# Kernel optimization log

Measured on AMD Instinct MI355X. Metric: run time of the kernel, lower is better.

## Reference

```python
import jax, jax.numpy as jnp
import numpy as np

WIN = 16
HEADS = 8


def _rel_index(win):
    c = np.stack(np.meshgrid(np.arange(win), np.arange(win), indexing='ij'), 0).reshape(2, -1)
    rel = (c[:, :, None] - c[:, None, :]).transpose(1, 2, 0) + win - 1
    return jnp.asarray(rel[..., 0] * (2 * win - 1) + rel[..., 1])


def setup_inputs() -> dict:
    key = jax.random.key(0)
    ks = jax.random.split(key, 10)
    B, H, W, C = 4, 128, 128, 256
    f = lambda k, s: jax.random.normal(k, s, dtype=jnp.float32)
    return {
        'x_wsa': f(ks[0], (B, H, W, C)),
        'x_original': f(ks[1], (B, H, W, C)),
        'q_w': f(ks[2], (C, C)) * 0.02,
        'q_b': f(ks[3], (C,)) * 0.02,
        'kv_w': f(ks[4], (5, 5, C // HEADS, 2 * C)) * 0.02,  # HWIO, grouped conv
        'kv_b': f(ks[5], (2 * C,)) * 0.02,
        'out_w': f(ks[6], (C, C)) * 0.02,
        'out_b': f(ks[7], (C,)) * 0.02,
        'bias_table': f(ks[8], ((2 * WIN - 1) ** 2, HEADS)) * 0.02,
        'rezero': jnp.full((1,), 0.5, dtype=jnp.float32),  # nonzero so output is informative
    }


def reference(x_wsa, x_original, q_w, q_b, kv_w, kv_b, out_w, out_b, bias_table, rezero):
    B, H, W, C = x_wsa.shape
    win, h = WIN, HEADS
    d = C // h
    nH, nW = H // win, W // win

    q = x_wsa @ q_w + q_b  # [B,H,W,C]
    kv = jax.lax.conv_general_dilated(
        x_original, kv_w, (1, 1), [(2, 2), (2, 2)],
        dimension_numbers=('NHWC', 'HWIO', 'NHWC'), feature_group_count=h) + kv_b  # [B,H,W,2C]

    def part(x):
        Cx = x.shape[-1]
        x = x.reshape(B, nH, win, nW, win, Cx).transpose(0, 1, 3, 2, 4, 5)
        return x.reshape(B * nH * nW, win * win, Cx)

    q = part(q)
    kv = part(kv)
    k, v = kv[..., :C], kv[..., C:]

    def heads(x):
        return x.reshape(x.shape[0], win * win, h, d).transpose(0, 2, 1, 3)

    q, k, v = heads(q), heads(k), heads(v)

    bias = bias_table[_rel_index(win)].transpose(2, 0, 1)
    scores = jnp.einsum('nhqd,nhkd->nhqk', q, k) * (1.0 / jnp.sqrt(jnp.asarray(d, q.dtype)))
    attn = jax.nn.softmax(scores + bias[None], axis=-1)
    o = jnp.einsum('nhqk,nhkd->nhqd', attn, v)

    # deheadify + reverse window partition
    o = o.transpose(0, 2, 1, 3).reshape(B, nH, nW, win, win, C)
    o = o.transpose(0, 1, 3, 2, 4, 5).reshape(B, H, W, C)
    return rezero * (o @ out_w + out_b)
```

## Files before the change

### kernel.cpp

```cpp
#include <hip/hip_runtime.h>
#include <math.h>

#define IMG 128
#define CDIM 256
#define NHEADS 8
#define DHEAD 32

typedef _Float16 half8 __attribute__((ext_vector_type(8)));
typedef _Float16 half4 __attribute__((ext_vector_type(4)));
typedef float floatx4 __attribute__((ext_vector_type(4)));

__global__ __launch_bounds__(256) void transpose_w_kernel(
    const float* __restrict__ w, _Float16* __restrict__ wT)
{
  const int n = blockIdx.x;
  const int k = threadIdx.x;
  wT[(size_t)n * 256 + k] = (_Float16)w[(size_t)k * 256 + n];
}

__global__ __launch_bounds__(512) void wt_kernel(const float* __restrict__ w,
                                                 _Float16* __restrict__ wT)
{
  const int tap = blockIdx.x;
  const int t = threadIdx.x;
  const int g = t >> 6, o = t & 63;
  _Float16 h[32];
#pragma unroll
  for (int ic = 0; ic < 32; ic++)
    h[ic] = (_Float16)w[(size_t)(tap * 32 + ic) * 512 + t];
  half8* dst = (half8*)(wT + (((size_t)g * 25 + tap) * 64 + o) * 32);
#pragma unroll
  for (int i = 0; i < 4; i++) dst[i] = *(half8*)(h + i * 8);
}

#define GSTR 40

template <bool AF16, bool OUTF16>
__global__ __launch_bounds__(256) void gemm_mfma_kernel(
    const void* __restrict__ Ap, const _Float16* __restrict__ BT,
    const float* __restrict__ bias, const float* __restrict__ scale_ptr,
    void* __restrict__ Cp)
{
  __shared__ _Float16 As[128 * GSTR];
  __shared__ _Float16 Bs[128 * GSTR];

  const int tid = threadIdx.x;
  const int m0 = blockIdx.x * 128;
  const int n0 = blockIdx.y * 128;
  const int wave = tid >> 6, lane = tid & 63;
  const int lq = lane & 15, quad = lane >> 4;
  const int wm = (wave >> 1) * 64, wn = (wave & 1) * 64;

  floatx4 acc[4][4];
#pragma unroll
  for (int i = 0; i < 4; i++)
#pragma unroll
    for (int j = 0; j < 4; j++) acc[i][j] = (floatx4){0.f, 0.f, 0.f, 0.f};

  for (int kc = 0; kc < 8; kc++) {
    const int k0 = kc * 32;
    __syncthreads();
    if (AF16) {
      const _Float16* A = (const _Float16*)Ap;
#pragma unroll
      for (int r = 0; r < 2; r++) {
        int idx = tid + r * 256;
        int row = idx >> 2, c8 = (idx & 3) * 8;
        *(half8*)(As + row * GSTR + c8) =
            *(const half8*)(A + (size_t)(m0 + row) * 256 + k0 + c8);
      }
    } else {
      const float* A = (const float*)Ap;
#pragma unroll
      for (int r = 0; r < 4; r++) {
        int idx = tid + r * 256;
        int row = idx >> 3, c4 = (idx & 7) * 4;
        float4 v = *(const float4*)(A + (size_t)(m0 + row) * 256 + k0 + c4);
        half4 h;
        h[0] = (_Float16)v.x; h[1] = (_Float16)v.y;
        h[2] = (_Float16)v.z; h[3] = (_Float16)v.w;
        *(half4*)(As + row * GSTR + c4) = h;
      }
    }
#pragma unroll
    for (int r = 0; r < 2; r++) {
      int idx = tid + r * 256;
      int row = idx >> 2, c8 = (idx & 3) * 8;
      *(half8*)(Bs + row * GSTR + c8) =
          *(const half8*)(BT + (size_t)(n0 + row) * 256 + k0 + c8);
    }
    __syncthreads();

    half8 aF[4], bF[4];
#pragma unroll
    for (int i = 0; i < 4; i++) {
      aF[i] = *(const half8*)(As + (wm + i * 16 + lq) * GSTR + quad * 8);
      bF[i] = *(const half8*)(Bs + (wn + i * 16 + lq) * GSTR + quad * 8);
    }
#pragma unroll
    for (int mt = 0; mt < 4; mt++)
#pragma unroll
      for (int nt = 0; nt < 4; nt++)
        acc[mt][nt] = __builtin_amdgcn_mfma_f32_16x16x32_f16(
            aF[mt], bF[nt], acc[mt][nt], 0, 0, 0);
  }

  const float s = scale_ptr ? scale_ptr[0] : 1.0f;
#pragma unroll
  for (int nt = 0; nt < 4; nt++) {
    const int n = n0 + wn + nt * 16 + lq;
    const float bv = bias[n];
#pragma unroll
    for (int mt = 0; mt < 4; mt++) {
      const int mbase = m0 + wm + mt * 16 + quad * 4;
#pragma unroll
      for (int r = 0; r < 4; r++) {
        float val = s * (acc[mt][nt][r] + bv);
        if (OUTF16)
          ((_Float16*)Cp)[(size_t)(mbase + r) * 256 + n] = (_Float16)val;
        else
          ((float*)Cp)[(size_t)(mbase + r) * 256 + n] = val;
      }
    }
  }
}

#define PS 40
#define PW 20

__global__ __launch_bounds__(256, 4) void conv_mfma_kernel(
    const float* __restrict__ xin, const _Float16* __restrict__ wT,
    const float* __restrict__ bias, _Float16* __restrict__ kvout)
{
  __shared__ _Float16 patch[400 * PS];

  const int tid  = threadIdx.x;
  const int tile = blockIdx.x;
  const int g    = blockIdx.y;
  const int b    = blockIdx.z;
  const int ty0 = (tile >> 3) * 16, tx0 = (tile & 7) * 16;

  for (int idx = tid; idx < 800; idx += 256) {
    int pix = idx >> 1, c0 = (idx & 1) * 16;
    int py = pix / 20, px = pix - py * 20;
    int gy = ty0 + py - 2, gx = tx0 + px - 2;
    _Float16 h[16];
    if ((unsigned)gy < (unsigned)IMG && (unsigned)gx < (unsigned)IMG) {
      const float4* src = (const float4*)(xin + ((((size_t)b * IMG + gy) * IMG) + gx) * CDIM + g * 32 + c0);
#pragma unroll
      for (int i = 0; i < 4; i++) {
        float4 v = src[i];
        h[i * 4 + 0] = (_Float16)v.x; h[i * 4 + 1] = (_Float16)v.y;
        h[i * 4 + 2] = (_Float16)v.z; h[i * 4 + 3] = (_Float16)v.w;
      }
    } else {
#pragma unroll
      for (int i = 0; i < 16; i++) h[i] = (_Float16)0.f;
    }
    *(half8*)(patch + pix * PS + c0)     = *(half8*)h;
    *(half8*)(patch + pix * PS + c0 + 8) = *(half8*)(h + 8);
  }

  const int wave = tid >> 6, lane = tid & 63;
  const int lq = lane & 15, quad = lane >> 4;

  floatx4 acc[4][4];
#pragma unroll
  for (int i = 0; i < 4; i++)
#pragma unroll
    for (int j = 0; j < 4; j++) acc[i][j] = (floatx4){0.f, 0.f, 0.f, 0.f};

  const _Float16* wg = wT + (size_t)g * 25 * 64 * 32 + (size_t)lq * 32 + quad * 8;

  __syncthreads();

  for (int ky = 0; ky < 5; ky++) {
#pragma unroll
    for (int kx = 0; kx < 5; kx++) {
      half8 bfr[4];
#pragma unroll
      for (int nt = 0; nt < 4; nt++) {
        int py = wave * 4 + nt + ky;
        bfr[nt] = *(const half8*)(patch + (py * PW + lq + kx) * PS + quad * 8);
      }
      const _Float16* wk = wg + (size_t)((ky * 5 + kx) * 64) * 32;
#pragma unroll
      for (int mt = 0; mt < 4; mt++) {
        half8 afr = *(const half8*)(wk + mt * 16 * 32);
#pragma unroll
        for (int nt = 0; nt < 4; nt++)
          acc[mt][nt] = __builtin_amdgcn_mfma_f32_16x16x32_f16(afr, bfr[nt], acc[mt][nt], 0, 0, 0);
      }
    }
  }

#pragma unroll
  for (int mt = 0; mt < 4; mt++) {
    float4 bv = *(const float4*)(bias + g * 64 + mt * 16 + quad * 4);
#pragma unroll
    for (int nt = 0; nt < 4; nt++) {
      int oy = ty0 + wave * 4 + nt;
      int ox = tx0 + lq;
      half4 ov;
      ov[0] = (_Float16)(acc[mt][nt][0] + bv.x);
      ov[1] = (_Float16)(acc[mt][nt][1] + bv.y);
      ov[2] = (_Float16)(acc[mt][nt][2] + bv.z);
      ov[3] = (_Float16)(acc[mt][nt][3] + bv.w);
      *(half4*)(kvout + ((((size_t)b * IMG + oy) * IMG) + ox) * 512 + g * 64 + mt * 16 + quad * 4) = ov;
    }
  }
}

#define KSTR 40
#define VSTR 264

__global__ __launch_bounds__(256, 3) void attn_mfma_kernel(
    _Float16* __restrict__ qf, const _Float16* __restrict__ kv,
    const float* __restrict__ bias_table)
{
  __shared__ _Float16 Kl[256 * KSTR];
  __shared__ _Float16 Vt[32 * VSTR];
  __shared__ float bsm[961];

  const int tid = threadIdx.x;
  const int n  = blockIdx.x;
  const int hh = blockIdx.y;
  const int b  = n >> 6;
  const int wy = (n >> 3) & 7;
  const int wx = n & 7;
  const int y0 = wy * 16, x0 = wx * 16;

  for (int i = tid; i < 961; i += 256) bsm[i] = bias_table[i * 8 + hh];

  {
    const int ty = tid >> 4, tx = tid & 15;
    size_t base = ((((size_t)b * IMG + y0 + ty) * IMG) + x0 + tx) * 512;
    const half8* kp = (const half8*)(kv + base + hh * 32);
    const half8* vp = (const half8*)(kv + base + 256 + hh * 32);
#pragma unroll
    for (int i = 0; i < 4; i++)
      *(half8*)(Kl + tid * KSTR + i * 8) = kp[i];
    half8 vh[4];
#pragma unroll
    for (int i = 0; i < 4; i++) vh[i] = vp[i];
#pragma unroll
    for (int i = 0; i < 4; i++)
#pragma unroll
      for (int j = 0; j < 8; j++)
        Vt[(i * 8 + j) * VSTR + tid] = vh[i][j];
  }

  const int wave = tid >> 6, lane = tid & 63;
  const int lq = lane & 15, quad = lane >> 4;

  half8 qB[4];
  int qbase[4];
  size_t qptr[4];
#pragma unroll
  for (int qt = 0; qt < 4; qt++) {
    int tok = wave * 64 + qt * 16 + lq;
    int qy = tok >> 4, qx = tok & 15;
    qbase[qt] = (qy + 15) * 31 + (qx + 15);
    size_t p = ((((size_t)b * IMG + y0 + qy) * IMG) + x0 + qx) * CDIM + hh * 32;
    qptr[qt] = p;
    qB[qt] = *(const half8*)(qf + p + quad * 8);
  }

  __syncthreads();

  float m[4] = {-1e30f, -1e30f, -1e30f, -1e30f};
  float l[4] = {0.f, 0.f, 0.f, 0.f};
  floatx4 Ot[2][4];
#pragma unroll
  for (int dt = 0; dt < 2; dt++)
#pragma unroll
    for (int qt = 0; qt < 4; qt++) Ot[dt][qt] = (floatx4){0.f, 0.f, 0.f, 0.f};

  const float scale = 0.17677669529663687f;

  for (int ch = 0; ch < 8; ch++) {
    half8 kA[2];
#pragma unroll
    for (int kt = 0; kt < 2; kt++)
      kA[kt] = *(const half8*)(Kl + (ch * 32 + kt * 16 + lq) * KSTR + quad * 8);

    floatx4 S[4][2];
#pragma unroll
    for (int qt = 0; qt < 4; qt++)
#pragma unroll
      for (int kt = 0; kt < 2; kt++)
        S[qt][kt] = __builtin_amdgcn_mfma_f32_16x16x32_f16(
            kA[kt], qB[qt], (floatx4){0.f, 0.f, 0.f, 0.f}, 0, 0, 0);

    half4 vA[2][2];
#pragma unroll
    for (int dt = 0; dt < 2; dt++)
#pragma unroll
      for (int kt = 0; kt < 2; kt++)
        vA[dt][kt] = *(const half4*)(Vt + (dt * 16 + lq) * VSTR +
                                     ch * 32 + kt * 16 + quad * 4);

    half4 pB[4][2];
#pragma unroll
    for (int qt = 0; qt < 4; qt++) {
      float sv[8];
#pragma unroll
      for (int kt = 0; kt < 2; kt++) {
        int keybase = ch * 32 + kt * 16 + quad * 4;
        int koff = (keybase >> 4) * 31 + (keybase & 15);
#pragma unroll
        for (int r = 0; r < 4; r++)
          sv[kt * 4 + r] = S[qt][kt][r] * scale + bsm[qbase[qt] - koff - r];
      }
      float mx = sv[0];
#pragma unroll
      for (int i = 1; i < 8; i++) mx = fmaxf(mx, sv[i]);
      mx = fmaxf(mx, __shfl_xor(mx, 16));
      mx = fmaxf(mx, __shfl_xor(mx, 32));
      float mn = fmaxf(m[qt], mx);
      float c = __expf(m[qt] - mn);
      m[qt] = mn;
      float ps = 0.f;
#pragma unroll
      for (int i = 0; i < 8; i++) { sv[i] = __expf(sv[i] - mn); ps += sv[i]; }
      ps += __shfl_xor(ps, 16);
      ps += __shfl_xor(ps, 32);
      l[qt] = l[qt] * c + ps;
#pragma unroll
      for (int dt = 0; dt < 2; dt++) {
        Ot[dt][qt][0] *= c; Ot[dt][qt][1] *= c;
        Ot[dt][qt][2] *= c; Ot[dt][qt][3] *= c;
      }
#pragma unroll
      for (int kt = 0; kt < 2; kt++) {
        half4 p4;
        p4[0] = (_Float16)sv[kt * 4 + 0]; p4[1] = (_Float16)sv[kt * 4 + 1];
        p4[2] = (_Float16)sv[kt * 4 + 2]; p4[3] = (_Float16)sv[kt * 4 + 3];
        pB[qt][kt] = p4;
      }
    }

#pragma unroll
    for (int qt = 0; qt < 4; qt++)
#pragma unroll
      for (int dt = 0; dt < 2; dt++)
#pragma unroll
        for (int kt = 0; kt < 2; kt++)
          Ot[dt][qt] = __builtin_amdgcn_mfma_f32_16x16x16f16(
              vA[dt][kt], pB[qt][kt], Ot[dt][qt], 0, 0, 0);
  }

#pragma unroll
  for (int qt = 0; qt < 4; qt++) {
    float inv = 1.0f / l[qt];
#pragma unroll
    for (int dt = 0; dt < 2; dt++) {
      half4 ov;
      ov[0] = (_Float16)(Ot[dt][qt][0] * inv);
      ov[1] = (_Float16)(Ot[dt][qt][1] * inv);
      ov[2] = (_Float16)(Ot[dt][qt][2] * inv);
      ov[3] = (_Float16)(Ot[dt][qt][3] * inv);
      *(half4*)(qf + qptr[qt] + dt * 16 + quad * 4) = ov;
    }
  }
}

extern "C" void kernel_launch(void* const* d_in, const int* in_sizes, int n_in,
                              void* d_out, int out_size, void* d_ws, size_t ws_size,
                              hipStream_t stream) {
  const float* x_wsa      = (const float*)d_in[0];
  const float* x_orig     = (const float*)d_in[1];
  const float* q_w        = (const float*)d_in[2];
  const float* q_b        = (const float*)d_in[3];
  const float* kv_w       = (const float*)d_in[4];
  const float* kv_b       = (const float*)d_in[5];
  const float* out_w      = (const float*)d_in[6];
  const float* out_b      = (const float*)d_in[7];
  const float* bias_table = (const float*)d_in[8];
  const float* rezero     = (const float*)d_in[9];
  float* out = (float*)d_out;

  _Float16* qf    = (_Float16*)d_ws;
  _Float16* kvbuf = (_Float16*)((char*)d_ws + 33554432);
  _Float16* wTc   = (_Float16*)((char*)d_ws + 100663296);
  _Float16* qwT   = (_Float16*)((char*)d_ws + 101711872);
  _Float16* owT   = (_Float16*)((char*)d_ws + 101974016);

  transpose_w_kernel<<<256, 256, 0, stream>>>(q_w, qwT);
  transpose_w_kernel<<<256, 256, 0, stream>>>(out_w, owT);
  wt_kernel<<<25, 512, 0, stream>>>(kv_w, wTc);

  gemm_mfma_kernel<false, true><<<dim3(512, 2), 256, 0, stream>>>(
      x_wsa, qwT, q_b, nullptr, qf);

  conv_mfma_kernel<<<dim3(64, 8, 4), 256, 0, stream>>>(x_orig, wTc, kv_b, kvbuf);

  attn_mfma_kernel<<<dim3(256, 8), 256, 0, stream>>>(qf, kvbuf, bias_table);

  gemm_mfma_kernel<true, false><<<dim3(512, 2), 256, 0, stream>>>(
      qf, owT, out_b, rezero, out);
}
```

Before: 349.1 us.

## Stage full B panel in LDS once, load A fragments directly from global

The GEMM kernel now loads the whole 128x256 weight panel into shared memory once at kernel start and removes the per-k-chunk A/B staging and its barriers. A fragments are read straight from global memory into registers (converting fp32 to fp16 in place), so the per-iteration syncthreads go away. The conv kernel's patch stride shrinks from 40 to 32 and its occupancy hint rises to 6 blocks per CU. Risks: larger LDS use in the GEMM limits occupancy, direct global A loads are less coalesced, and the unpadded conv stride may add LDS bank conflicts.

```diff
diff --git a/kernel.cpp b/kernel.cpp
--- a/kernel.cpp
+++ b/kernel.cpp
@@ -33,16 +33,15 @@
   for (int i = 0; i < 4; i++) dst[i] = *(half8*)(h + i * 8);
 }
 
-#define GSTR 40
+#define BSTR 264
 
 template <bool AF16, bool OUTF16>
-__global__ __launch_bounds__(256) void gemm_mfma_kernel(
+__global__ __launch_bounds__(256, 2) void gemm_mfma_kernel(
     const void* __restrict__ Ap, const _Float16* __restrict__ BT,
     const float* __restrict__ bias, const float* __restrict__ scale_ptr,
     void* __restrict__ Cp)
 {
-  __shared__ _Float16 As[128 * GSTR];
-  __shared__ _Float16 Bs[128 * GSTR];
+  __shared__ _Float16 Bs[128 * BSTR];
 
   const int tid = threadIdx.x;
   const int m0 = blockIdx.x * 128;
@@ -51,52 +50,52 @@
   const int lq = lane & 15, quad = lane >> 4;
   const int wm = (wave >> 1) * 64, wn = (wave & 1) * 64;
 
+#pragma unroll
+  for (int r = 0; r < 16; r++) {
+    int idx = tid + r * 256;
+    int row = idx >> 5, c8 = (idx & 31) * 8;
+    *(half8*)(Bs + row * BSTR + c8) =
+        *(const half8*)(BT + (size_t)(n0 + row) * 256 + c8);
+  }
+  __syncthreads();
+
   floatx4 acc[4][4];
 #pragma unroll
   for (int i = 0; i < 4; i++)
 #pragma unroll
     for (int j = 0; j < 4; j++) acc[i][j] = (floatx4){0.f, 0.f, 0.f, 0.f};
 
+#pragma unroll
   for (int kc = 0; kc < 8; kc++) {
     const int k0 = kc * 32;
-    __syncthreads();
+
+    half8 aF[4];
     if (AF16) {
       const _Float16* A = (const _Float16*)Ap;
 #pragma unroll
-      for (int r = 0; r < 2; r++) {
-        int idx = tid + r * 256;
-        int row = idx >> 2, c8 = (idx & 3) * 8;
-        *(half8*)(As + row * GSTR + c8) =
-            *(const half8*)(A + (size_t)(m0 + row) * 256 + k0 + c8);
-      }
+      for (int i = 0; i < 4; i++)
+        aF[i] = *(const half8*)(A + (size_t)(m0 + wm + i * 16 + lq) * 256 + k0 + quad * 8);
     } else {
       const float* A = (const float*)Ap;
 #pragma unroll
-      for (int r = 0; r < 4; r++) {
-        int idx = tid + r * 256;
-        int row = idx >> 3, c4 = (idx & 7) * 4;
-        float4 v = *(const float4*)(A + (size_t)(m0 + row) * 256 + k0 + c4);
-        half4 h;
-        h[0] = (_Float16)v.x; h[1] = (_Float16)v.y;
-        h[2] = (_Float16)v.z; h[3] = (_Float16)v.w;
-        *(half4*)(As + row * GSTR + c4) = h;
-      }
-    }
-#pragma unroll
-    for (int r = 0; r < 2; r++) {
-      int idx = tid + r * 256;
-      int row = idx >> 2, c8 = (idx & 3) * 8;
-      *(half8*)(Bs + row * GSTR + c8) =
-          *(const half8*)(BT + (size_t)(n0 + row) * 256 + k0 + c8);
-    }
-    __syncthreads();
-
-    half8 aF[4], bF[4];
-#pragma unroll
-    for (int i = 0; i < 4; i++) {
-      aF[i] = *(const half8*)(As + (wm + i * 16 + lq) * GSTR + quad * 8);
-      bF[i] = *(const half8*)(Bs + (wn + i * 16 + lq) * GSTR + quad * 8);
-    }
+      for (int i = 0; i < 4; i++) {
+        const float* p = A + (size_t)(m0 + wm + i * 16 + lq) * 256 + k0 + quad * 8;
+        float4 v0 = *(const float4*)(p);
+        float4 v1 = *(const float4*)(p + 4);
+        half8 h;
+        h[0] = (_Float16)v0.x; h[1] = (_Float16)v0.y;
+        h[2] = (_Float16)v0.z; h[3] = (_Float16)v0.w;
+        h[4] = (_Float16)v1.x; h[5] = (_Float16)v1.y;
+        h[6] = (_Float16)v1.z; h[7] = (_Float16)v1.w;
+        aF[i] = h;
+      }
+    }
+
+    half8 bF[4];
+#pragma unroll
+    for (int i = 0; i < 4; i++)
+      bF[i] = *(const half8*)(Bs + (wn + i * 16 + lq) * BSTR + k0 + quad * 8);
+
 #pragma unroll
     for (int mt = 0; mt < 4; mt++)
 #pragma unroll
@@ -125,10 +124,10 @@
   }
 }
 
-#define PS 40
+#define PS 32
 #define PW 20
 
-__global__ __launch_bounds__(256, 4) void conv_mfma_kernel(
+__global__ __launch_bounds__(256, 6) void conv_mfma_kernel(
     const float* __restrict__ xin, const _Float16* __restrict__ wT,
     const float* __restrict__ bias, _Float16* __restrict__ kvout)
 {
```

Measured after the change: 932.2 us. +167.0%, slower.
